# Kernel optimization log

Measured on AMD Instinct MI355X. Metric: run time of the kernel, lower is better.

Reference implementation:

```python
import jax, jax.numpy as jnp
import numpy as np

B, S, D, H = 2, 2048, 1024, 16
HD = D // H  # 64
NEG = 1.0e9


def setup_inputs() -> dict:
    key = jax.random.key(0)
    ks = jax.random.split(key, 9)
    scale = 1.0 / np.sqrt(D)
    return {
        "q_in": jax.random.normal(ks[0], (B, S, D), jnp.float32),
        "k_in": jax.random.normal(ks[1], (B, S, D), jnp.float32),
        "v_in": jax.random.normal(ks[2], (B, S, D), jnp.float32),
        "Wq": jax.random.normal(ks[3], (D, D), jnp.float32) * scale,
        "bq": jnp.zeros((D,), jnp.float32),
        "Wk": jax.random.normal(ks[4], (D, D), jnp.float32) * scale,
        "bk": jnp.zeros((D,), jnp.float32),
        "Wv": jax.random.normal(ks[5], (D, D), jnp.float32) * scale,
        "bv": jnp.zeros((D,), jnp.float32),
        "Wo": jax.random.normal(ks[6], (D, D), jnp.float32) * scale,
        "bo": jnp.zeros((D,), jnp.float32),
    }


def _split_heads(x):
    # [B,S,D] -> [B,H,S,HD]
    return x.reshape(B, S, H, HD).transpose(0, 2, 1, 3)


def reference(q_in, k_in, v_in, Wq, bq, Wk, bk, Wv, bv, Wo, bo):
    q = _split_heads(q_in @ Wq + bq)
    k = _split_heads(k_in @ Wk + bk)
    v = _split_heads(v_in @ Wv + bv)
    # scaled dot-product attention with additive causal mask (use_causal_mask=True)
    scores = jnp.einsum("bhqd,bhkd->bhqk", q, k) / jnp.sqrt(jnp.float32(HD))
    causal = jnp.tril(jnp.ones((S, S), jnp.float32))  # band_part(ones, -1, 0)
    scores = scores + (causal - 1.0) * NEG
    weights = jax.nn.softmax(scores, axis=-1)
    attn = jnp.einsum("bhqk,bhkd->bhqd", weights, v)
    concat = attn.transpose(0, 2, 1, 3).reshape(B, S, D)
    return concat @ Wo + bo
```

## Files before the change

kernel.cpp:

```cpp
#include <hip/hip_runtime.h>

#define B_  2
#define S_  2048
#define D_  1024
#define H_  16
#define HD_ 64
#define MM  (B_ * S_)

typedef __bf16 bf16;
typedef __attribute__((ext_vector_type(8))) __bf16 bf16x8;
typedef __attribute__((ext_vector_type(4))) __bf16 bf16x4;
typedef __attribute__((ext_vector_type(4))) float  f32x4;

__device__ inline float exp2g(float x) { return __builtin_amdgcn_exp2f(x); }

__device__ inline bf16x8 load8(const bf16* p) { return *(const bf16x8*)p; }
__device__ inline bf16x8 load8(const float* p) {
  float4 a = *(const float4*)p;
  float4 b = *(const float4*)(p + 4);
  bf16x8 r;
  r[0] = (bf16)a.x; r[1] = (bf16)a.y; r[2] = (bf16)a.z; r[3] = (bf16)a.w;
  r[4] = (bf16)b.x; r[5] = (bf16)b.y; r[6] = (bf16)b.z; r[7] = (bf16)b.w;
  return r;
}

__device__ inline void gld16(void* lds, const void* g) {
  __builtin_amdgcn_global_load_lds(
      (const __attribute__((address_space(1))) unsigned int*)g,
      (__attribute__((address_space(3))) unsigned int*)lds, 16, 0, 0);
}

__global__ __launch_bounds__(256) void transpose_w(
    const float* __restrict__ W0, const float* __restrict__ W1,
    const float* __restrict__ W2, const float* __restrict__ W3,
    bf16* __restrict__ T0, bf16* __restrict__ T1,
    bf16* __restrict__ T2, bf16* __restrict__ T3,
    const float* __restrict__ X0, const float* __restrict__ X1,
    const float* __restrict__ X2,
    bf16* __restrict__ Y0, bf16* __restrict__ Y1, bf16* __restrict__ Y2) {
  const int z = blockIdx.z;
  if (z >= 4) {
    const int p = z - 4, t = p >> 2;
    const float* src = t == 0 ? X0 : t == 1 ? X1 : X2;
    bf16* dst = t == 0 ? Y0 : t == 1 ? Y1 : Y2;
    long base = ((long)(p & 3) << 20) +
                (long)(blockIdx.y * 32 + blockIdx.x) * 1024 + threadIdx.x * 4;
    float4 v = *(const float4*)&src[base];
    bf16x4 o4;
    o4[0] = (bf16)v.x; o4[1] = (bf16)v.y; o4[2] = (bf16)v.z; o4[3] = (bf16)v.w;
    *(bf16x4*)&dst[base] = o4;
    return;
  }
  __shared__ bf16 t[32][40];
  const float* in = z == 0 ? W0 : z == 1 ? W1 : z == 2 ? W2 : W3;
  bf16* out = z == 0 ? T0 : z == 1 ? T1 : z == 2 ? T2 : T3;
  const int tx = threadIdx.x & 31;
  const int ty = threadIdx.x >> 5;
  const int r0 = blockIdx.y * 32, c0 = blockIdx.x * 32;
#pragma unroll
  for (int j = 0; j < 32; j += 8)
    t[ty + j][tx] = (bf16)in[(long)(r0 + ty + j) * D_ + (c0 + tx)];
  __syncthreads();
#pragma unroll
  for (int j = 0; j < 32; j += 8)
    out[(long)(c0 + ty + j) * D_ + (r0 + tx)] = t[tx][ty + j];
}

__global__ __launch_bounds__(256) void transpose_v64(const bf16* __restrict__ V,
                                                     bf16* __restrict__ VT) {
  __shared__ bf16 t[64][72];
  const int tid = threadIdx.x;
  const int s0 = blockIdx.x * 64;
  const int bh = blockIdx.y;
  const int b = bh >> 4, h = bh & 15;
  const bf16* ip = V + (long)b * S_ * D_ + h * HD_;
  bf16* op = VT + (long)bh * HD_ * S_;
#pragma unroll
  for (int i = 0; i < 2; ++i) {
    int c = tid + i * 256;
    int r = c >> 3, cc = (c & 7) * 8;
    *(bf16x8*)&t[r][cc] = *(const bf16x8*)&ip[(long)(s0 + r) * D_ + cc];
  }
  __syncthreads();
#pragma unroll
  for (int i = 0; i < 2; ++i) {
    int c = tid + i * 256;
    int d = c >> 3, sc = (c & 7) * 8;
    bf16x8 v;
#pragma unroll
    for (int j = 0; j < 8; ++j) v[j] = t[sc + j][d];
    *(bf16x8*)&op[(long)d * S_ + s0 + sc] = v;
  }
}

template <typename AT, typename OT>
__global__ __launch_bounds__(256) void gemm_bt_dma(
    const AT* __restrict__ A0, const AT* __restrict__ A1, const AT* __restrict__ A2,
    const bf16* __restrict__ B0, const bf16* __restrict__ B1, const bf16* __restrict__ B2,
    const float* __restrict__ c0, const float* __restrict__ c1, const float* __restrict__ c2,
    OT* __restrict__ C0, OT* __restrict__ C1, OT* __restrict__ C2,
    int M, int N, int K) {
  __shared__ bf16 lA[2][128][32];
  __shared__ bf16 lB[2][128][32];
  const int z = blockIdx.z;
  const AT*    A    = z == 0 ? A0 : z == 1 ? A1 : A2;
  const bf16*  Bt   = z == 0 ? B0 : z == 1 ? B1 : B2;
  const float* bias = z == 0 ? c0 : z == 1 ? c1 : c2;
  OT*          C    = z == 0 ? C0 : z == 1 ? C1 : C2;

  const int tid = threadIdx.x;
  const int lane = tid & 63, wave = tid >> 6;
  const int quad = lane >> 4, l16 = lane & 15;
  const int id = blockIdx.x + (blockIdx.y << 3);
  const int nid = (id & 7) * 32 + (id >> 3);
  const int bm = (nid >> 3) * 128, bn = (nid & 7) * 128;
  const int wm = (wave >> 1) * 64, wn = (wave & 1) * 64;

  f32x4 acc[4][4] = {};

  for (int k0 = 0; k0 < K; k0 += 64) {
    __syncthreads();
#pragma unroll
    for (int hh = 0; hh < 2; ++hh) {
#pragma unroll
      for (int i = 0; i < 2; ++i) {
        const int nbase = wave * 128 + i * 64;
        const int n = nbase + lane;
        const int row = n >> 2, kc = (n & 3) * 8;
        gld16(&lB[hh][0][0] + (long)nbase * 8,
              &Bt[(long)(bn + row) * K + k0 + hh * 32 + kc]);
        if constexpr (__is_same(AT, bf16))
          gld16(&lA[hh][0][0] + (long)nbase * 8,
                &A[(long)(bm + row) * K + k0 + hh * 32 + kc]);
      }
      if constexpr (!__is_same(AT, bf16)) {
#pragma unroll
        for (int i = 0; i < 2; ++i) {
          int c = tid + i * 256;
          int row = c >> 2, kc = (c & 3) * 8;
          *(bf16x8*)&lA[hh][row][kc] =
              load8(&A[(long)(bm + row) * K + k0 + hh * 32 + kc]);
        }
      }
    }
    __syncthreads();
#pragma unroll
    for (int hh = 0; hh < 2; ++hh) {
      bf16x8 af[4], bfr[4];
#pragma unroll
      for (int i = 0; i < 4; ++i) {
        af[i]  = *(const bf16x8*)&lA[hh][wm + i * 16 + l16][quad * 8];
        bfr[i] = *(const bf16x8*)&lB[hh][wn + i * 16 + l16][quad * 8];
      }
#pragma unroll
      for (int mi = 0; mi < 4; ++mi)
#pragma unroll
        for (int ni = 0; ni < 4; ++ni)
          acc[mi][ni] = __builtin_amdgcn_mfma_f32_16x16x32_bf16(
              af[mi], bfr[ni], acc[mi][ni], 0, 0, 0);
    }
  }

#pragma unroll
  for (int mi = 0; mi < 4; ++mi)
#pragma unroll
    for (int ni = 0; ni < 4; ++ni) {
      int col = bn + wn + ni * 16 + l16;
      float bv = bias[col];
#pragma unroll
      for (int r = 0; r < 4; ++r) {
        int row = bm + wm + mi * 16 + quad * 4 + r;
        C[(long)row * N + col] = (OT)(acc[mi][ni][r] + bv);
      }
    }
}

__global__ __launch_bounds__(256) void gemm_bt_64(const bf16* __restrict__ A,
                                                  const bf16* __restrict__ Bt,
                                                  const float* __restrict__ bias,
                                                  float* __restrict__ C,
                                                  int M, int N, int K) {
  __shared__ bf16 lA[2][128][32];
  __shared__ bf16 lB[2][64][32];
  const int tid = threadIdx.x;
  const int lane = tid & 63, wave = tid >> 6;
  const int quad = lane >> 4, l16 = lane & 15;
  const int id = blockIdx.x + (blockIdx.y << 4);
  const int nid = (id & 7) * 64 + (id >> 3);
  const int bm = (nid >> 4) * 128, bn = (nid & 15) * 64;
  const int wm = (wave >> 1) * 64, wn = (wave & 1) * 32;

  f32x4 acc[4][2] = {};

  for (int k0 = 0; k0 < K; k0 += 64) {
    __syncthreads();
#pragma unroll
    for (int hh = 0; hh < 2; ++hh) {
#pragma unroll
      for (int i = 0; i < 2; ++i) {
        const int nbase = wave * 128 + i * 64;
        const int n = nbase + lane;
        const int row = n >> 2, kc = (n & 3) * 8;
        gld16(&lA[hh][0][0] + (long)nbase * 8,
              &A[(long)(bm + row) * K + k0 + hh * 32 + kc]);
      }
      {
        const int nbase = wave * 64;
        const int n = nbase + lane;
        const int row = n >> 2, kc = (n & 3) * 8;
        gld16(&lB[hh][0][0] + (long)nbase * 8,
              &Bt[(long)(bn + row) * K + k0 + hh * 32 + kc]);
      }
    }
    __syncthreads();
#pragma unroll
    for (int hh = 0; hh < 2; ++hh) {
      bf16x8 af[4], bfr[2];
#pragma unroll
      for (int i = 0; i < 4; ++i)
        af[i] = *(const bf16x8*)&lA[hh][wm + i * 16 + l16][quad * 8];
#pragma unroll
      for (int i = 0; i < 2; ++i)
        bfr[i] = *(const bf16x8*)&lB[hh][wn + i * 16 + l16][quad * 8];
#pragma unroll
      for (int mi = 0; mi < 4; ++mi)
#pragma unroll
        for (int ni = 0; ni < 2; ++ni)
          acc[mi][ni] = __builtin_amdgcn_mfma_f32_16x16x32_bf16(
              af[mi], bfr[ni], acc[mi][ni], 0, 0, 0);
    }
  }

#pragma unroll
  for (int mi = 0; mi < 4; ++mi)
#pragma unroll
    for (int ni = 0; ni < 2; ++ni) {
      int col = bn + wn + ni * 16 + l16;
      float bv = bias[col];
#pragma unroll
      for (int r = 0; r < 4; ++r) {
        int row = bm + wm + mi * 16 + quad * 4 + r;
        C[(long)row * N + col] = acc[mi][ni][r] + bv;
      }
    }
}

#define SCALE_LOG2E 0.1803368801111244f

__device__ inline void attn_step5(bool diag, int qloc, int quad, int l16,
                                  const bf16 (*lKb)[64], const bf16 (*lVb)[64],
                                  bf16 (*lpw)[72], const bf16x8* aq,
                                  f32x4* o, float& l_s) {
  const int sw = l16 & 7;
  f32x4 s[4];
#pragma unroll
  for (int ni = 0; ni < 4; ++ni) {
    f32x4 a = {};
#pragma unroll
    for (int c = 0; c < 2; ++c) {
      bf16x8 kf = *(const bf16x8*)&lKb[ni * 16 + l16][((c * 4 + quad) ^ sw) * 8];
      a = __builtin_amdgcn_mfma_f32_16x16x32_bf16(kf, aq[c], a, 0, 0, 0);
    }
    s[ni] = a * SCALE_LOG2E;
  }
  if (diag) {
#pragma unroll
    for (int ni = 0; ni < 4; ++ni)
#pragma unroll
      for (int r = 0; r < 4; ++r)
        if (ni * 16 + quad * 4 + r > qloc) s[ni][r] = -1e9f;
  }
  float rs = 0.f;
#pragma unroll
  for (int ni = 0; ni < 4; ++ni) {
    bf16x4 p4;
#pragma unroll
    for (int r = 0; r < 4; ++r) {
      float p = exp2g(s[ni][r]);
      p4[r] = (bf16)p;
      rs += p;
    }
    *(bf16x4*)&lpw[l16][ni * 16 + quad * 4] = p4;
  }
  l_s += rs;
#pragma unroll
  for (int c = 0; c < 2; ++c) {
    bf16x8 ap = *(const bf16x8*)&lpw[l16][c * 32 + quad * 8];
#pragma unroll
    for (int di = 0; di < 4; ++di) {
      bf16x8 vf = *(const bf16x8*)&lVb[di * 16 + l16][((c * 4 + quad) ^ sw) * 8];
      o[di] = __builtin_amdgcn_mfma_f32_16x16x32_bf16(vf, ap, o[di], 0, 0, 0);
    }
  }
}

__device__ inline void store_o(bf16* Ob, int qrow, int lane, int quad, int l16,
                               bf16 (*lpw)[72], const f32x4* o, float l_s) {
  float rs = l_s;
  rs += __shfl_xor(rs, 16);
  rs += __shfl_xor(rs, 32);
  const float inv = 1.0f / rs;
#pragma unroll
  for (int di = 0; di < 4; ++di) {
    bf16x4 p4;
#pragma unroll
    for (int r = 0; r < 4; ++r) p4[r] = (bf16)(o[di][r] * inv);
    *(bf16x4*)&lpw[l16][di * 16 + quad * 4] = p4;
  }
  const int q = lane >> 2, db = (lane & 3) * 16;
  bf16x8 v0 = *(const bf16x8*)&lpw[q][db];
  bf16x8 v1 = *(const bf16x8*)&lpw[q][db + 8];
  *(bf16x8*)&Ob[(long)(qrow + q) * D_ + db] = v0;
  *(bf16x8*)&Ob[(long)(qrow + q) * D_ + db + 8] = v1;
}

__global__ __launch_bounds__(512) void flash_attn8(const bf16* __restrict__ Q,
                                                   const bf16* __restrict__ K,
                                                   const bf16* __restrict__ VT,
                                                   bf16* __restrict__ O) {
  __shared__ bf16 lK[2][64][64];
  __shared__ bf16 lV[2][64][64];
  __shared__ bf16 lp[8][16][72];
  const int tid = threadIdx.x;
  const int lane = tid & 63, wave = tid >> 6;
  const int quad = lane >> 4, l16 = lane & 15;
  const int x = blockIdx.x, bh = blockIdx.y;
  const bool flip = (bh & 16) != 0;
  const int qtA = flip ? 30 - 2 * x : 2 * x;
  const int qtB = qtA + 1;
  const bool isB = wave >= 4;
  const int w4 = wave & 3;
  const int myqt = isB ? qtB : qtA;
  const int b = bh >> 4, h = bh & 15;
  const bf16* Qb = Q + (long)b * S_ * D_ + h * HD_;
  const bf16* Kb = K + (long)b * S_ * D_ + h * HD_;
  const bf16* Vb = VT + (long)bh * HD_ * S_;
  const int qrow = myqt * 64 + w4 * 16;
  const int qloc = w4 * 16 + l16;

  bf16x8 aq[2];
#pragma unroll
  for (int c = 0; c < 2; ++c)
    aq[c] = *(const bf16x8*)&Qb[(long)(qrow + l16) * D_ + c * 32 + quad * 8];

  f32x4 o[4] = {};
  float l_s = 0.f;

  const int srow = tid >> 3, scol = tid & 7;
  const int swcol = (scol ^ (srow & 7)) * 8;
  const int ktMax = qtB;

  bf16x8 rkA, rvA, rkB, rvB;
  rkA = *(const bf16x8*)&Kb[(long)srow * D_ + scol * 8];
  rvA = *(const bf16x8*)&Vb[(long)srow * S_ + scol * 8];
  *(bf16x8*)&lK[0][srow][swcol] = rkA;
  *(bf16x8*)&lV[0][srow][swcol] = rvA;
  rkA = *(const bf16x8*)&Kb[(long)(64 + srow) * D_ + scol * 8];
  rvA = *(const bf16x8*)&Vb[(long)srow * S_ + 64 + scol * 8];
  __syncthreads();

  for (int kt = 0; kt < ktMax; kt += 2) {
    if (kt + 2 <= ktMax) {
      const long k0 = (long)(kt + 2) * 64;
      rkB = *(const bf16x8*)&Kb[(k0 + srow) * D_ + scol * 8];
      rvB = *(const bf16x8*)&Vb[(long)srow * S_ + k0 + scol * 8];
    }
    if (isB || kt <= qtA)
      attn_step5(kt == myqt, qloc, quad, l16, lK[0], lV[0], lp[wave], aq,
                 o, l_s);
    *(bf16x8*)&lK[1][srow][swcol] = rkA;
    *(bf16x8*)&lV[1][srow][swcol] = rvA;
    __syncthreads();
    if (kt + 3 <= ktMax) {
      const long k0 = (long)(kt + 3) * 64;
      rkA = *(const bf16x8*)&Kb[(k0 + srow) * D_ + scol * 8];
      rvA = *(const bf16x8*)&Vb[(long)srow * S_ + k0 + scol * 8];
    }
    if (isB || kt + 1 <= qtA)
      attn_step5(kt + 1 == myqt, qloc, quad, l16, lK[1], lV[1], lp[wave], aq,
                 o, l_s);
    if (kt + 1 < ktMax) {
      *(bf16x8*)&lK[0][srow][swcol] = rkB;
      *(bf16x8*)&lV[0][srow][swcol] = rvB;
      __syncthreads();
    }
  }

  bf16* Ob = O + (long)b * S_ * D_ + h * HD_;
  store_o(Ob, qrow, lane, quad, l16, lp[wave], o, l_s);
}

extern "C" void kernel_launch(void* const* d_in, const int* in_sizes, int n_in,
                              void* d_out, int out_size, void* d_ws, size_t ws_size,
                              hipStream_t stream) {
  (void)in_sizes; (void)n_in; (void)out_size;
  const float* q_in = (const float*)d_in[0];
  const float* k_in = (const float*)d_in[1];
  const float* v_in = (const float*)d_in[2];
  const float* Wq   = (const float*)d_in[3];
  const float* bq   = (const float*)d_in[4];
  const float* Wk   = (const float*)d_in[5];
  const float* bk   = (const float*)d_in[6];
  const float* Wv   = (const float*)d_in[7];
  const float* bv   = (const float*)d_in[8];
  const float* Wo   = (const float*)d_in[9];
  const float* bo   = (const float*)d_in[10];
  float* out = (float*)d_out;

  bf16* ws = (bf16*)d_ws;
  const size_t WSZ = (size_t)D_ * D_;
  const size_t TSZ = (size_t)B_ * S_ * D_;
  bf16* WqT = ws;
  bf16* WkT = WqT + WSZ;
  bf16* WvT = WkT + WSZ;
  bf16* WoT = WvT + WSZ;
  bf16* Qp  = WoT + WSZ;
  bf16* Kp  = Qp + TSZ;
  bf16* Vp  = Kp + TSZ;
  bf16* VTp = Vp + TSZ;
  bf16* Ap  = VTp + TSZ;
  bf16* Xq  = VTp;
  bf16* Xk  = Ap;
  bf16* Xv  = Ap + TSZ;
  const bool pre = ws_size >= (4 * WSZ + 6 * TSZ) * sizeof(bf16);

  dim3 blk(256);
  transpose_w<<<dim3(32, 32, pre ? 16 : 4), blk, 0, stream>>>(
      Wq, Wk, Wv, Wo, WqT, WkT, WvT, WoT, q_in, k_in, v_in, Xq, Xk, Xv);

  if (pre)
    gemm_bt_dma<bf16, bf16><<<dim3(8, 32, 3), blk, 0, stream>>>(
        Xq, Xk, Xv, WqT, WkT, WvT, bq, bk, bv, Qp, Kp, Vp, MM, D_, D_);
  else
    gemm_bt_dma<float, bf16><<<dim3(8, 32, 3), blk, 0, stream>>>(
        q_in, k_in, v_in, WqT, WkT, WvT, bq, bk, bv, Qp, Kp, Vp, MM, D_, D_);

  transpose_v64<<<dim3(S_ / 64, B_ * H_), blk, 0, stream>>>(Vp, VTp);

  flash_attn8<<<dim3(16, B_ * H_), dim3(512), 0, stream>>>(Qp, Kp, VTp, Ap);

  gemm_bt_64<<<dim3(16, 32), blk, 0, stream>>>(Ap, WoT, bo, out, MM, D_, D_);
}
```

Measured before the change: 205.3 us.

## Double-buffer GEMM LDS tiles to overlap global loads with MFMA compute

Both projection GEMM kernels switch from loading a 64-wide K slab into two LDS halves and then computing, to a ping-pong pipeline over 32-wide K tiles. The next tile is prefetched into the other buffer while MFMAs run on the current one, with one barrier per iteration. This is meant to hide global-load latency behind compute. The cost is twice as many loop iterations with smaller work per barrier. For fp32 A inputs the register-staged conversion loads still block before their LDS stores.

```diff
diff --git a/kernel.cpp b/kernel.cpp
--- a/kernel.cpp
+++ b/kernel.cpp
@@ -117,49 +117,52 @@
   const int wm = (wave >> 1) * 64, wn = (wave & 1) * 64;
 
   f32x4 acc[4][4] = {};
-
-  for (int k0 = 0; k0 < K; k0 += 64) {
+  const int NT = K >> 5;
+
+#define STAGE_DMA(buf, t)                                                    \
+  {                                                                          \
+    const int k0 = (t) << 5;                                                 \
+    _Pragma("unroll") for (int i = 0; i < 2; ++i) {                          \
+      const int nbase = wave * 128 + i * 64;    \
+      const int n = nbase + lane;                                            \
+      const int row = n >> 2, kc = (n & 3) * 8;                              \
+      gld16(&lB[buf][0][0] + (long)nbase * 8,                                \
+            &Bt[(long)(bn + row) * K + k0 + kc]);                            \
+      if constexpr (__is_same(AT, bf16))                                     \
+        gld16(&lA[buf][0][0] + (long)nbase * 8,                              \
+              &A[(long)(bm + row) * K + k0 + kc]);                           \
+    }                                                                        \
+    if constexpr (!__is_same(AT, bf16)) {                                    \
+      _Pragma("unroll") for (int i = 0; i < 2; ++i) {                        \
+        int cch = tid + i * 256;                                             \
+        int row = cch >> 2, kc = (cch & 3) * 8;                              \
+        *(bf16x8*)&lA[buf][row][kc] =                                        \
+            load8(&A[(long)(bm + row) * K + k0 + kc]);                       \
+      }                                                                      \
+    }                                                                        \
+  }
+
+  STAGE_DMA(0, 0);
+  __syncthreads();
+
+  for (int t = 0; t < NT; ++t) {
+    const int buf = t & 1;
+    if (t + 1 < NT) STAGE_DMA(buf ^ 1, t + 1);
+    bf16x8 af[4], bfr[4];
+#pragma unroll
+    for (int i = 0; i < 4; ++i) {
+      af[i]  = *(const bf16x8*)&lA[buf][wm + i * 16 + l16][quad * 8];
+      bfr[i] = *(const bf16x8*)&lB[buf][wn + i * 16 + l16][quad * 8];
+    }
+#pragma unroll
+    for (int mi = 0; mi < 4; ++mi)
+#pragma unroll
+      for (int ni = 0; ni < 4; ++ni)
+        acc[mi][ni] = __builtin_amdgcn_mfma_f32_16x16x32_bf16(
+            af[mi], bfr[ni], acc[mi][ni], 0, 0, 0);
     __syncthreads();
-#pragma unroll
-    for (int hh = 0; hh < 2; ++hh) {
-#pragma unroll
-      for (int i = 0; i < 2; ++i) {
-        const int nbase = wave * 128 + i * 64;
-        const int n = nbase + lane;
-        const int row = n >> 2, kc = (n & 3) * 8;
-        gld16(&lB[hh][0][0] + (long)nbase * 8,
-              &Bt[(long)(bn + row) * K + k0 + hh * 32 + kc]);
-        if constexpr (__is_same(AT, bf16))
-          gld16(&lA[hh][0][0] + (long)nbase * 8,
-                &A[(long)(bm + row) * K + k0 + hh * 32 + kc]);
-      }
-      if constexpr (!__is_same(AT, bf16)) {
-#pragma unroll
-        for (int i = 0; i < 2; ++i) {
-          int c = tid + i * 256;
-          int row = c >> 2, kc = (c & 3) * 8;
-          *(bf16x8*)&lA[hh][row][kc] =
-              load8(&A[(long)(bm + row) * K + k0 + hh * 32 + kc]);
-        }
-      }
-    }
-    __syncthreads();
-#pragma unroll
-    for (int hh = 0; hh < 2; ++hh) {
-      bf16x8 af[4], bfr[4];
-#pragma unroll
-      for (int i = 0; i < 4; ++i) {
-        af[i]  = *(const bf16x8*)&lA[hh][wm + i * 16 + l16][quad * 8];
-        bfr[i] = *(const bf16x8*)&lB[hh][wn + i * 16 + l16][quad * 8];
-      }
-#pragma unroll
-      for (int mi = 0; mi < 4; ++mi)
-#pragma unroll
-        for (int ni = 0; ni < 4; ++ni)
-          acc[mi][ni] = __builtin_amdgcn_mfma_f32_16x16x32_bf16(
-              af[mi], bfr[ni], acc[mi][ni], 0, 0, 0);
-    }
-  }
+  }
+#undef STAGE_DMA
 
 #pragma unroll
   for (int mi = 0; mi < 4; ++mi)
@@ -191,45 +194,49 @@
   const int wm = (wave >> 1) * 64, wn = (wave & 1) * 32;
 
   f32x4 acc[4][2] = {};
-
-  for (int k0 = 0; k0 < K; k0 += 64) {
+  const int NT = K >> 5;
+
+#define STAGE64(buf, t)                                                      \
+  {                                                                          \
+    const int k0 = (t) << 5;                                                 \
+    _Pragma("unroll") for (int i = 0; i < 2; ++i) {                          \
+      const int nbase = wave * 128 + i * 64;                                 \
+      const int n = nbase + lane;                                            \
+      const int row = n >> 2, kc = (n & 3) * 8;                              \
+      gld16(&lA[buf][0][0] + (long)nbase * 8,                                \
+            &A[(long)(bm + row) * K + k0 + kc]);                             \
+    }                                                                        \
+    {                                                                        \
+      const int nbase = wave * 64;                                           \
+      const int n = nbase + lane;                                            \
+      const int row = n >> 2, kc = (n & 3) * 8;                              \
+      gld16(&lB[buf][0][0] + (long)nbase * 8,                                \
+            &Bt[(long)(bn + row) * K + k0 + kc]);                            \
+    }                                                                        \
+  }
+
+  STAGE64(0, 0);
+  __syncthreads();
+
+  for (int t = 0; t < NT; ++t) {
+    const int buf = t & 1;
+    if (t + 1 < NT) STAGE64(buf ^ 1, t + 1);
+    bf16x8 af[4], bfr[2];
+#pragma unroll
+    for (int i = 0; i < 4; ++i)
+      af[i] = *(const bf16x8*)&lA[buf][wm + i * 16 + l16][quad * 8];
+#pragma unroll
+    for (int i = 0; i < 2; ++i)
+      bfr[i] = *(const bf16x8*)&lB[buf][wn + i * 16 + l16][quad * 8];
+#pragma unroll
+    for (int mi = 0; mi < 4; ++mi)
+#pragma unroll
+      for (int ni = 0; ni < 2; ++ni)
+        acc[mi][ni] = __builtin_amdgcn_mfma_f32_16x16x32_bf16(
+            af[mi], bfr[ni], acc[mi][ni], 0, 0, 0);
     __syncthreads();
-#pragma unroll
-    for (int hh = 0; hh < 2; ++hh) {
-#pragma unroll
-      for (int i = 0; i < 2; ++i) {
-        const int nbase = wave * 128 + i * 64;
-        const int n = nbase + lane;
-        const int row = n >> 2, kc = (n & 3) * 8;
-        gld16(&lA[hh][0][0] + (long)nbase * 8,
-              &A[(long)(bm + row) * K + k0 + hh * 32 + kc]);
-      }
-      {
-        const int nbase = wave * 64;
-        const int n = nbase + lane;
-        const int row = n >> 2, kc = (n & 3) * 8;
-        gld16(&lB[hh][0][0] + (long)nbase * 8,
-              &Bt[(long)(bn + row) * K + k0 + hh * 32 + kc]);
-      }
-    }
-    __syncthreads();
-#pragma unroll
-    for (int hh = 0; hh < 2; ++hh) {
-      bf16x8 af[4], bfr[2];
-#pragma unroll
-      for (int i = 0; i < 4; ++i)
-        af[i] = *(const bf16x8*)&lA[hh][wm + i * 16 + l16][quad * 8];
-#pragma unroll
-      for (int i = 0; i < 2; ++i)
-        bfr[i] = *(const bf16x8*)&lB[hh][wn + i * 16 + l16][quad * 8];
-#pragma unroll
-      for (int mi = 0; mi < 4; ++mi)
-#pragma unroll
-        for (int ni = 0; ni < 2; ++ni)
-          acc[mi][ni] = __builtin_amdgcn_mfma_f32_16x16x32_bf16(
-              af[mi], bfr[ni], acc[mi][ni], 0, 0, 0);
-    }
-  }
+  }
+#undef STAGE64
 
 #pragma unroll
   for (int mi = 0; mi < 4; ++mi)
```

Result: slower. 212.3 us (+3.4%).
